# Performance work log

Measured on AMD Instinct MI355X. Metric: run time of the kernel, lower is better.

Reference implementation:

```python
import jax, jax.numpy as jnp
import numpy as np

N_NODES = 100000


def gcn_conv(x, edge_index, W, b, n_nodes):
    """PyG GCNConv: linear -> add self-loops -> symmetric-normalized scatter-sum -> bias."""
    h = x @ W  # [N, F_out]
    loop = jnp.arange(n_nodes, dtype=edge_index.dtype)
    src = jnp.concatenate([edge_index[0], loop])
    dst = jnp.concatenate([edge_index[1], loop])
    # degree of destination nodes (self-loops included)
    deg = jax.ops.segment_sum(jnp.ones_like(dst, dtype=h.dtype), dst, num_segments=n_nodes)
    dinv = jnp.where(deg > 0, jax.lax.rsqrt(deg), 0.0)
    norm = dinv[src] * dinv[dst]  # [E+N]
    msg = h[src] * norm[:, None]  # gather + scale
    out = jax.ops.segment_sum(msg, dst, num_segments=n_nodes)  # scatter-add
    return out + b


def setup_inputs() -> dict:
    key = jax.random.key(0)
    k1, k2, k3, k4 = jax.random.split(key, 4)
    d_in, hidden, out = 128, 256, 64
    x = jax.random.normal(k1, (N_NODES, d_in), dtype=jnp.float32)
    edge_index = jax.random.randint(k2, (2, 800000), 0, N_NODES, dtype=jnp.int64)
    W1 = jax.random.normal(k3, (d_in, hidden), dtype=jnp.float32) * (1.0 / np.sqrt(d_in))
    b1 = jnp.zeros((hidden,), dtype=jnp.float32)
    W2 = jax.random.normal(k4, (hidden, out), dtype=jnp.float32) * (1.0 / np.sqrt(hidden))
    b2 = jnp.zeros((out,), dtype=jnp.float32)
    return {"x": x, "edge_index": edge_index, "W1": W1, "b1": b1, "W2": W2, "b2": b2}


def reference(x, edge_index, W1, b1, W2, b2):
    h = jax.nn.relu(gcn_conv(x, edge_index, W1, b1, N_NODES))
    # dropout p=0 (module default) -> identity
    return gcn_conv(h, edge_index, W2, b2, N_NODES)
```

## Files before the change

### kernel.cpp

```cpp
#include <hip/hip_runtime.h>
#include <hip/hip_bf16.h>

#define N_NODES 100000
#define D_IN 128
#define HID 256
#define D_OUT 64
#define TR 32
#define NBUK 196
#define BSH 9

typedef __attribute__((ext_vector_type(8))) short bf8;
typedef __attribute__((ext_vector_type(4))) float f4;

static __device__ __forceinline__ unsigned short f2bf(float f) {
    __hip_bfloat16 h = __float2bfloat16(f);
    return *reinterpret_cast<unsigned short*>(&h);
}
static __device__ __forceinline__ float bflo(unsigned int u) { return __uint_as_float(u << 16); }
static __device__ __forceinline__ float bfhi(unsigned int u) { return __uint_as_float(u & 0xffff0000u); }

static __device__ __forceinline__ void fma8(float* a, float w, uint4 u) {
    a[0] += w * bflo(u.x); a[1] += w * bfhi(u.x);
    a[2] += w * bflo(u.y); a[3] += w * bfhi(u.y);
    a[4] += w * bflo(u.z); a[5] += w * bfhi(u.z);
    a[6] += w * bflo(u.w); a[7] += w * bfhi(u.w);
}
static __device__ __forceinline__ void fma4(float* a, float w, uint2 u) {
    a[0] += w * bflo(u.x); a[1] += w * bfhi(u.x);
    a[2] += w * bflo(u.y); a[3] += w * bfhi(u.y);
}


__global__ __launch_bounds__(256) void k_prep(const float* __restrict__ x,
                                              unsigned long long* __restrict__ xb,
                                              const float* __restrict__ W1,
                                              unsigned short* __restrict__ W1t,
                                              const float* __restrict__ W2,
                                              unsigned short* __restrict__ W2t,
                                              const int* __restrict__ dst, int E,
                                              int* __restrict__ hist2d) {
    int b = blockIdx.x, t = threadIdx.x;
    if (b < 12500) {
        int i = b * 256 + t;
        float4 v = ((const float4*)x)[i];
        unsigned long long o = (unsigned long long)f2bf(v.x) |
                               ((unsigned long long)f2bf(v.y) << 16) |
                               ((unsigned long long)f2bf(v.z) << 32) |
                               ((unsigned long long)f2bf(v.w) << 48);
        xb[i] = o;
    } else if (b < 12628) {
        int i = (b - 12500) * 256 + t;
        int n = i >> 7, k = i & 127;
        W1t[i] = f2bf(W1[k * HID + n]);
    } else if (b < 12692) {
        int i = (b - 12628) * 256 + t;
        int n = i >> 8, k = i & 255;
        W2t[i] = f2bf(W2[k * D_OUT + n]);
    } else {
        int hb = b - 12692;
        __shared__ int h[NBUK];
        if (t < NBUK) h[t] = 0;
        __syncthreads();
        int base = hb * 4096;
        for (int j = 0; j < 16; j++) {
            int e = base + j * 256 + t;
            if (e < E) atomicAdd(&h[dst[e] >> BSH], 1);
        }
        __syncthreads();
        if (t < NBUK) hist2d[hb * NBUK + t] = h[t];
    }
}


__global__ __launch_bounds__(256) void k_scanB1(const int* __restrict__ hist2d,
                                                int* __restrict__ blockbase,
                                                int* __restrict__ bsumB, int nbb) {
    __shared__ int s[256];
    int u = blockIdx.x, t = threadIdx.x;
    int v = (t < nbb) ? hist2d[t * NBUK + u] : 0;
    s[t] = v;
    __syncthreads();
    for (int off = 1; off < 256; off <<= 1) {
        int w = (t >= off) ? s[t - off] : 0;
        __syncthreads();
        s[t] += w;
        __syncthreads();
    }
    if (t < nbb) blockbase[t * NBUK + u] = s[t] - v;
    if (t == 255) bsumB[u] = s[255];
}

static __device__ __forceinline__ void bucket_scan(const int* __restrict__ bsumB,
                                                   int* s, int* exs, int t) {
    int v = (t < NBUK) ? bsumB[t] : 0;
    s[t] = v;
    __syncthreads();
    for (int off = 1; off < 256; off <<= 1) {
        int w = (t >= off) ? s[t - off] : 0;
        __syncthreads();
        s[t] += w;
        __syncthreads();
    }
    if (t < NBUK) exs[t] = s[t] - v;
    if (t == NBUK - 1) exs[NBUK] = s[t];
    __syncthreads();
}


__global__ __launch_bounds__(256) void k_bin(const int* __restrict__ src,
                                             const int* __restrict__ dst, int E,
                                             const int* __restrict__ blockbase,
                                             const int* __restrict__ bsumB,
                                             unsigned int* __restrict__ bin) {
    __shared__ int s[256], exs[NBUK + 1];
    __shared__ int baseL[NBUK], rankL[NBUK];
    int t = threadIdx.x;
    bucket_scan(bsumB, s, exs, t);
    if (t < NBUK) {
        baseL[t] = exs[t] + blockbase[blockIdx.x * NBUK + t];
        rankL[t] = 0;
    }
    __syncthreads();
    int base = blockIdx.x * 4096;
    for (int j = 0; j < 16; j++) {
        int e = base + j * 256 + t;
        if (e < E) {
            int sv = src[e], d = dst[e];
            int bu = d >> BSH;
            int r = atomicAdd(&rankL[bu], 1);
            bin[baseL[bu] + r] = ((unsigned int)(d & 511) << 17) | (unsigned int)sv;
        }
    }
}


__global__ __launch_bounds__(256) void k_cntscan(const unsigned int* __restrict__ bin,
                                                 const int* __restrict__ bsumB,
                                                 int* __restrict__ row_ptr,
                                                 float* __restrict__ dinv) {
    __shared__ int sb[256], exs[NBUK + 1];
    __shared__ int c[512];
    __shared__ int s[256];
    int b = blockIdx.x, t = threadIdx.x;
    bucket_scan(bsumB, sb, exs, t);
    int lo = exs[b], hi = exs[b + 1];
    c[t] = 0;
    c[t + 256] = 0;
    __syncthreads();
    for (int e = lo + t; e < hi; e += 256) atomicAdd(&c[bin[e] >> 17], 1);
    __syncthreads();
    int a0 = c[2 * t], a1 = c[2 * t + 1];
    s[t] = a0 + a1;
    __syncthreads();
    for (int off = 1; off < 256; off <<= 1) {
        int u = (t >= off) ? s[t - off] : 0;
        __syncthreads();
        s[t] += u;
        __syncthreads();
    }
    int ex = (t > 0) ? s[t - 1] : 0;
    int n0 = (b << BSH) + 2 * t;
    if (n0 < N_NODES) {
        row_ptr[n0] = lo + ex;
        dinv[n0] = rsqrtf((float)a0 + 1.0f);
    }
    if (n0 + 1 < N_NODES) {
        row_ptr[n0 + 1] = lo + ex + a0;
        dinv[n0 + 1] = rsqrtf((float)a1 + 1.0f);
    }
    if (b == NBUK - 1 && t == 255) row_ptr[N_NODES] = exs[NBUK];
}


__global__ __launch_bounds__(256) void k_place(const unsigned int* __restrict__ bin,
                                               const int* __restrict__ bsumB,
                                               const int* __restrict__ row_ptr,
                                               const float* __restrict__ dinv,
                                               int2* __restrict__ cw) {
    __shared__ int sb[256], exs[NBUK + 1];
    __shared__ int cur[512];
    __shared__ float dl[512];
    int b = blockIdx.x, t = threadIdx.x;
    bucket_scan(bsumB, sb, exs, t);
    int node0 = b << BSH;
    int nbn = N_NODES - node0;
    if (nbn > 512) nbn = 512;
    if (t < nbn) {
        cur[t] = row_ptr[node0 + t];
        dl[t] = dinv[node0 + t];
    }
    if (t + 256 < nbn) {
        cur[t + 256] = row_ptr[node0 + t + 256];
        dl[t + 256] = dinv[node0 + t + 256];
    }
    __syncthreads();
    int lo = exs[b], hi = exs[b + 1];
    for (int e = lo + t; e < hi; e += 256) {
        unsigned int rec = bin[e];
        int sv = rec & 0x1FFFF;
        int dloc = rec >> 17;
        int pos = atomicAdd(&cur[dloc], 1);
        int2 v;
        v.x = sv;
        v.y = __float_as_int(dinv[sv] * dl[dloc]);
        cw[pos] = v;
    }
}


__global__ __launch_bounds__(256) void k_pull1m(const int* __restrict__ row_ptr,
                                                const int2* __restrict__ cw,
                                                const uint4* __restrict__ xb4,
                                                const float* __restrict__ dinv,
                                                const unsigned short* __restrict__ W1t,
                                                const float* __restrict__ b1,
                                                const unsigned short* __restrict__ W2t,
                                                unsigned short* __restrict__ mb) {
    __shared__ char sA[TR * 256];
    __shared__ char sH[TR * 512];
    int t = threadIdx.x, wave = t >> 6, lane = t & 63;
    int g = lane >> 4, l = lane & 15;
    size_t row0 = (size_t)blockIdx.x * TR;

    for (int r = 0; r < 2; r++) {
        int row = r * 16 + wave * 4 + g;
        int node = (int)row0 + row;
        int beg = row_ptr[node], end = row_ptr[node + 1];
        float di = dinv[node];
        float a[8] = {0, 0, 0, 0, 0, 0, 0, 0};
        fma8(a, di * di, xb4[(size_t)node * 16 + l]);
        int e = beg;
        if (e + 4 <= end) {
            int2 c0 = cw[e], c1 = cw[e + 1], c2 = cw[e + 2], c3 = cw[e + 3];
            uint4 u0 = xb4[(size_t)c0.x * 16 + l];
            uint4 u1 = xb4[(size_t)c1.x * 16 + l];
            uint4 u2 = xb4[(size_t)c2.x * 16 + l];
            uint4 u3 = xb4[(size_t)c3.x * 16 + l];
            e += 4;
            for (; e + 4 <= end; e += 4) {
                int2 d0 = cw[e], d1 = cw[e + 1], d2 = cw[e + 2], d3 = cw[e + 3];
                uint4 v0 = xb4[(size_t)d0.x * 16 + l];
                uint4 v1 = xb4[(size_t)d1.x * 16 + l];
                uint4 v2 = xb4[(size_t)d2.x * 16 + l];
                uint4 v3 = xb4[(size_t)d3.x * 16 + l];
                fma8(a, __int_as_float(c0.y), u0);
                fma8(a, __int_as_float(c1.y), u1);
                fma8(a, __int_as_float(c2.y), u2);
                fma8(a, __int_as_float(c3.y), u3);
                c0 = d0; c1 = d1; c2 = d2; c3 = d3;
                u0 = v0; u1 = v1; u2 = v2; u3 = v3;
            }
            fma8(a, __int_as_float(c0.y), u0);
            fma8(a, __int_as_float(c1.y), u1);
            fma8(a, __int_as_float(c2.y), u2);
            fma8(a, __int_as_float(c3.y), u3);
        }
        for (; e < end; e++) {
            int2 c = cw[e];
            fma8(a, __int_as_float(c.y), xb4[(size_t)c.x * 16 + l]);
        }
        uint4 o;
        o.x = (unsigned int)f2bf(a[0]) | ((unsigned int)f2bf(a[1]) << 16);
        o.y = (unsigned int)f2bf(a[2]) | ((unsigned int)f2bf(a[3]) << 16);
        o.z = (unsigned int)f2bf(a[4]) | ((unsigned int)f2bf(a[5]) << 16);
        o.w = (unsigned int)f2bf(a[6]) | ((unsigned int)f2bf(a[7]) << 16);
        *(uint4*)(sA + ((row * 256 + l * 16) ^ ((row & 7) << 4))) = o;
    }
    __syncthreads();

    int lr = lane & 15, lg = lane >> 4;
#pragma unroll
    for (int th = 0; th < 2; th++) {
        bf8 w1f[4][2];
#pragma unroll
        for (int kk = 0; kk < 4; kk++)
#pragma unroll
            for (int q = 0; q < 2; q++)
                w1f[kk][q] = *(const bf8*)(W1t + (size_t)(wave * 64 + (th * 2 + q) * 16 + lr) * D_IN + kk * 32 + lg * 8);
        f4 acc[2][2];
#pragma unroll
        for (int q = 0; q < 2; q++) {
            acc[q][0] = (f4){0.f, 0.f, 0.f, 0.f};
            acc[q][1] = (f4){0.f, 0.f, 0.f, 0.f};
        }
#pragma unroll
        for (int kk = 0; kk < 4; kk++) {
            bf8 a0 = *(const bf8*)(sA + ((lr * 256 + kk * 64 + lg * 16) ^ ((lr & 7) << 4)));
            bf8 a1 = *(const bf8*)(sA + (((16 + lr) * 256 + kk * 64 + lg * 16) ^ (((16 + lr) & 7) << 4)));
#pragma unroll
            for (int q = 0; q < 2; q++) {
                acc[q][0] = __builtin_amdgcn_mfma_f32_16x16x32_bf16(a0, w1f[kk][q], acc[q][0], 0, 0, 0);
                acc[q][1] = __builtin_amdgcn_mfma_f32_16x16x32_bf16(a1, w1f[kk][q], acc[q][1], 0, 0, 0);
            }
        }
#pragma unroll
        for (int q = 0; q < 2; q++) {
            int colc = wave * 64 + (th * 2 + q) * 16 + lr;
            float bias = b1[colc];
#pragma unroll
            for (int h = 0; h < 2; h++) {
#pragma unroll
                for (int ri = 0; ri < 4; ri++) {
                    int row = h * 16 + lg * 4 + ri;
                    float hv = acc[q][h][ri] + bias;
                    hv = hv > 0.f ? hv : 0.f;
                    *(unsigned short*)(sH + ((row * 512 + colc * 2) ^ ((row & 7) << 4))) = f2bf(hv);
                }
            }
        }
    }
    __syncthreads();

    bf8 w2f[8];
#pragma unroll
    for (int kk = 0; kk < 8; kk++)
        w2f[kk] = *(const bf8*)(W2t + (size_t)(wave * 16 + lr) * HID + kk * 32 + lg * 8);
    f4 acc2[2];
    acc2[0] = (f4){0.f, 0.f, 0.f, 0.f};
    acc2[1] = (f4){0.f, 0.f, 0.f, 0.f};
#pragma unroll
    for (int kk = 0; kk < 8; kk++) {
        bf8 a0 = *(const bf8*)(sH + ((lr * 512 + kk * 64 + lg * 16) ^ ((lr & 7) << 4)));
        bf8 a1 = *(const bf8*)(sH + (((16 + lr) * 512 + kk * 64 + lg * 16) ^ (((16 + lr) & 7) << 4)));
        acc2[0] = __builtin_amdgcn_mfma_f32_16x16x32_bf16(a0, w2f[kk], acc2[0], 0, 0, 0);
        acc2[1] = __builtin_amdgcn_mfma_f32_16x16x32_bf16(a1, w2f[kk], acc2[1], 0, 0, 0);
    }
    int colc = wave * 16 + lr;
#pragma unroll
    for (int h = 0; h < 2; h++)
#pragma unroll
        for (int ri = 0; ri < 4; ri++) {
            int row = h * 16 + lg * 4 + ri;
            mb[(row0 + row) * D_OUT + colc] = f2bf(acc2[h][ri]);
        }
}


__global__ __launch_bounds__(256) void k_pull2(const int* __restrict__ row_ptr,
                                               const int2* __restrict__ cw,
                                               const uint2* __restrict__ m2,
                                               const float* __restrict__ dinv,
                                               const float* __restrict__ b2,
                                               float4* __restrict__ out4) {
    int wave = (blockIdx.x * 256 + threadIdx.x) >> 6;
    int lane = threadIdx.x & 63;
    int g = lane >> 4, l = lane & 15;
    int node = wave * 4 + g;
    int beg = row_ptr[node], end = row_ptr[node + 1];
    float di = dinv[node];
    float a[4] = {0, 0, 0, 0};
    fma4(a, di * di, m2[(size_t)node * 16 + l]);
    int e = beg;
    if (e + 4 <= end) {
        int2 c0 = cw[e], c1 = cw[e + 1], c2 = cw[e + 2], c3 = cw[e + 3];
        uint2 u0 = m2[(size_t)c0.x * 16 + l];
        uint2 u1 = m2[(size_t)c1.x * 16 + l];
        uint2 u2 = m2[(size_t)c2.x * 16 + l];
        uint2 u3 = m2[(size_t)c3.x * 16 + l];
        e += 4;
        for (; e + 4 <= end; e += 4) {
            int2 d0 = cw[e], d1 = cw[e + 1], d2 = cw[e + 2], d3 = cw[e + 3];
            uint2 v0 = m2[(size_t)d0.x * 16 + l];
            uint2 v1 = m2[(size_t)d1.x * 16 + l];
            uint2 v2 = m2[(size_t)d2.x * 16 + l];
            uint2 v3 = m2[(size_t)d3.x * 16 + l];
            fma4(a, __int_as_float(c0.y), u0);
            fma4(a, __int_as_float(c1.y), u1);
            fma4(a, __int_as_float(c2.y), u2);
            fma4(a, __int_as_float(c3.y), u3);
            c0 = d0; c1 = d1; c2 = d2; c3 = d3;
            u0 = v0; u1 = v1; u2 = v2; u3 = v3;
        }
        fma4(a, __int_as_float(c0.y), u0);
        fma4(a, __int_as_float(c1.y), u1);
        fma4(a, __int_as_float(c2.y), u2);
        fma4(a, __int_as_float(c3.y), u3);
    }
    for (; e < end; e++) {
        int2 c = cw[e];
        fma4(a, __int_as_float(c.y), m2[(size_t)c.x * 16 + l]);
    }
    float4 bv = ((const float4*)b2)[l];
    float4 o;
    o.x = a[0] + bv.x;
    o.y = a[1] + bv.y;
    o.z = a[2] + bv.z;
    o.w = a[3] + bv.w;
    out4[(size_t)node * 16 + l] = o;
}


extern "C" void kernel_launch(void* const* d_in, const int* in_sizes, int n_in,
                              void* d_out, int out_size, void* d_ws, size_t ws_size,
                              hipStream_t stream) {
    const float* x  = (const float*)d_in[0];
    const int*   ei = (const int*)d_in[1];
    const float* W1 = (const float*)d_in[2];
    const float* b1 = (const float*)d_in[3];
    const float* W2 = (const float*)d_in[4];
    const float* b2 = (const float*)d_in[5];
    float* out = (float*)d_out;

    const int E = in_sizes[1] / 2;
    const int* src = ei;
    const int* dst = ei + E;

    char* ws = (char*)d_ws;
    int* row_ptr        = (int*)(ws + 0);
    int2* cw            = (int2*)(ws + 400640);
    float* dinv         = (float*)(ws + 6800640);
    unsigned short* W1t = (unsigned short*)(ws + 7201024);
    unsigned short* W2t = (unsigned short*)(ws + 7266560);
    unsigned short* xb  = (unsigned short*)(ws + 7299328);
    unsigned short* mb  = (unsigned short*)(ws + 32899328);
    unsigned int* bin   = (unsigned int*)mb;
    int* hist2d         = (int*)((char*)mb + 3200256);
    int* blockbase      = (int*)((char*)mb + 3354112);
    int* bsumB          = (int*)((char*)mb + 3507968);

    const int NBB = (E + 4095) / 4096;

    k_prep<<<12692 + NBB, 256, 0, stream>>>(x, (unsigned long long*)xb, W1, W1t, W2, W2t,
                                            dst, E, hist2d);
    k_scanB1<<<NBUK, 256, 0, stream>>>(hist2d, blockbase, bsumB, NBB);
    k_bin<<<NBB, 256, 0, stream>>>(src, dst, E, blockbase, bsumB, bin);
    k_cntscan<<<NBUK, 256, 0, stream>>>(bin, bsumB, row_ptr, dinv);
    k_place<<<NBUK, 256, 0, stream>>>(bin, bsumB, row_ptr, dinv, cw);
    k_pull1m<<<3125, 256, 0, stream>>>(row_ptr, cw, (const uint4*)xb, dinv, W1t, b1, W2t, mb);
    k_pull2<<<6250, 256, 0, stream>>>(row_ptr, cw, (const uint2*)mb, dinv, b2, (float4*)out);
}
```

Baseline: 154.2 us.

## Split gather from MFMA stage and run persistent MFMA kernel reusing weights

The fused gather+MLP kernel is split in two. A standalone aggregation kernel writes bf16 aggregates to global memory, and a persistent MFMA kernel with 625 blocks loads W1/W2 fragments once and loops over five 32-row tiles, writing its 64-wide output in place into the 128-wide aggregate buffer. The gather loops are also rewritten as branchless 4-edge batches with masked weights, so there is no scalar tail loop. This trades an extra global round trip of the aggregates, plus an extra launch, for higher gather occupancy and fewer weight reloads.

```diff
diff --git a/kernel.cpp b/kernel.cpp
--- a/kernel.cpp
+++ b/kernel.cpp
@@ -8,6 +8,7 @@
 #define TR 32
 #define NBUK 196
 #define BSH 9
+#define MGRID 625
 
 typedef __attribute__((ext_vector_type(8))) short bf8;
 typedef __attribute__((ext_vector_type(4))) float f4;
@@ -28,6 +29,31 @@
 static __device__ __forceinline__ void fma4(float* a, float w, uint2 u) {
     a[0] += w * bflo(u.x); a[1] += w * bfhi(u.x);
     a[2] += w * bflo(u.y); a[3] += w * bfhi(u.y);
+}
+
+static __device__ __forceinline__ void loadb4(const int2* __restrict__ cw,
+                                              const uint4* __restrict__ xb4,
+                                              int e, int end, int beg, int l,
+                                              float* w, uint4* u) {
+#pragma unroll
+    for (int j = 0; j < 4; j++) {
+        int ej = (e + j < end) ? e + j : beg;
+        int2 c = cw[ej];
+        w[j] = (e + j < end) ? __int_as_float(c.y) : 0.f;
+        u[j] = xb4[(size_t)c.x * 16 + l];
+    }
+}
+static __device__ __forceinline__ void loadb2(const int2* __restrict__ cw,
+                                              const uint2* __restrict__ m2,
+                                              int e, int end, int beg, int l,
+                                              float* w, uint2* u) {
+#pragma unroll
+    for (int j = 0; j < 4; j++) {
+        int ej = (e + j < end) ? e + j : beg;
+        int2 c = cw[ej];
+        w[j] = (e + j < end) ? __int_as_float(c.y) : 0.f;
+        u[j] = m2[(size_t)c.x * 32 + l];
+    }
 }
 
 
@@ -208,131 +234,131 @@
 }
 
 
-__global__ __launch_bounds__(256) void k_pull1m(const int* __restrict__ row_ptr,
-                                                const int2* __restrict__ cw,
-                                                const uint4* __restrict__ xb4,
-                                                const float* __restrict__ dinv,
-                                                const unsigned short* __restrict__ W1t,
-                                                const float* __restrict__ b1,
-                                                const unsigned short* __restrict__ W2t,
-                                                unsigned short* __restrict__ mb) {
-    __shared__ char sA[TR * 256];
-    __shared__ char sH[TR * 512];
+__global__ __launch_bounds__(256) void k_pull1(const int* __restrict__ row_ptr,
+                                               const int2* __restrict__ cw,
+                                               const uint4* __restrict__ xb4,
+                                               const float* __restrict__ dinv,
+                                               uint4* __restrict__ agg4) {
+    int wave = (blockIdx.x * 256 + threadIdx.x) >> 6;
+    int lane = threadIdx.x & 63;
+    int g = lane >> 4, l = lane & 15;
+    int node = wave * 4 + g;
+    int beg = row_ptr[node], end = row_ptr[node + 1];
+    float di = dinv[node];
+    float a[8] = {0, 0, 0, 0, 0, 0, 0, 0};
+    fma8(a, di * di, xb4[(size_t)node * 16 + l]);
+    int cnt = end - beg;
+    if (cnt > 0) {
+        int nb = (cnt + 3) >> 2;
+        float w[4];
+        uint4 u[4];
+        loadb4(cw, xb4, beg, end, beg, l, w, u);
+        for (int b = 1; b < nb; b++) {
+            float nw[4];
+            uint4 nu[4];
+            loadb4(cw, xb4, beg + b * 4, end, beg, l, nw, nu);
+            fma8(a, w[0], u[0]);
+            fma8(a, w[1], u[1]);
+            fma8(a, w[2], u[2]);
+            fma8(a, w[3], u[3]);
+#pragma unroll
+            for (int j = 0; j < 4; j++) {
+                w[j] = nw[j];
+                u[j] = nu[j];
+            }
+        }
+        fma8(a, w[0], u[0]);
+        fma8(a, w[1], u[1]);
+        fma8(a, w[2], u[2]);
+        fma8(a, w[3], u[3]);
+    }
+    uint4 o;
+    o.x = (unsigned int)f2bf(a[0]) | ((unsigned int)f2bf(a[1]) << 16);
+    o.y = (unsigned int)f2bf(a[2]) | ((unsigned int)f2bf(a[3]) << 16);
+    o.z = (unsigned int)f2bf(a[4]) | ((unsigned int)f2bf(a[5]) << 16);
+    o.w = (unsigned int)f2bf(a[6]) | ((unsigned int)f2bf(a[7]) << 16);
+    agg4[(size_t)node * 16 + l] = o;
+}
+
+
+__global__ __launch_bounds__(256) void k_fused_mfma(unsigned short* __restrict__ agg,
+                                                    const unsigned short* __restrict__ W1t,
+                                                    const float* __restrict__ b1,
+                                                    const unsigned short* __restrict__ W2t) {
+    __shared__ char sH[TR * HID * 2];
     int t = threadIdx.x, wave = t >> 6, lane = t & 63;
-    int g = lane >> 4, l = lane & 15;
-    size_t row0 = (size_t)blockIdx.x * TR;
-
-    for (int r = 0; r < 2; r++) {
-        int row = r * 16 + wave * 4 + g;
-        int node = (int)row0 + row;
-        int beg = row_ptr[node], end = row_ptr[node + 1];
-        float di = dinv[node];
-        float a[8] = {0, 0, 0, 0, 0, 0, 0, 0};
-        fma8(a, di * di, xb4[(size_t)node * 16 + l]);
-        int e = beg;
-        if (e + 4 <= end) {
-            int2 c0 = cw[e], c1 = cw[e + 1], c2 = cw[e + 2], c3 = cw[e + 3];
-            uint4 u0 = xb4[(size_t)c0.x * 16 + l];
-            uint4 u1 = xb4[(size_t)c1.x * 16 + l];
-            uint4 u2 = xb4[(size_t)c2.x * 16 + l];
-            uint4 u3 = xb4[(size_t)c3.x * 16 + l];
-            e += 4;
-            for (; e + 4 <= end; e += 4) {
-                int2 d0 = cw[e], d1 = cw[e + 1], d2 = cw[e + 2], d3 = cw[e + 3];
-                uint4 v0 = xb4[(size_t)d0.x * 16 + l];
-                uint4 v1 = xb4[(size_t)d1.x * 16 + l];
-                uint4 v2 = xb4[(size_t)d2.x * 16 + l];
-                uint4 v3 = xb4[(size_t)d3.x * 16 + l];
-                fma8(a, __int_as_float(c0.y), u0);
-                fma8(a, __int_as_float(c1.y), u1);
-                fma8(a, __int_as_float(c2.y), u2);
-                fma8(a, __int_as_float(c3.y), u3);
-                c0 = d0; c1 = d1; c2 = d2; c3 = d3;
-                u0 = v0; u1 = v1; u2 = v2; u3 = v3;
+    int lr = lane & 15, lg = lane >> 4;
+
+    bf8 w1f[4][4];
+#pragma unroll
+    for (int kk = 0; kk < 4; kk++)
+#pragma unroll
+        for (int tt = 0; tt < 4; tt++)
+            w1f[kk][tt] = *(const bf8*)(W1t + (size_t)(wave * 64 + tt * 16 + lr) * D_IN + kk * 32 + lg * 8);
+    bf8 w2f[8];
+#pragma unroll
+    for (int kk = 0; kk < 8; kk++)
+        w2f[kk] = *(const bf8*)(W2t + (size_t)(wave * 16 + lr) * HID + kk * 32 + lg * 8);
+    float bias[4];
+#pragma unroll
+    for (int tt = 0; tt < 4; tt++) bias[tt] = b1[wave * 64 + tt * 16 + lr];
+
+    for (int it = 0; it < 5; it++) {
+        size_t row0 = ((size_t)blockIdx.x + (size_t)it * MGRID) * TR;
+
+        f4 acc1[4][2];
+#pragma unroll
+        for (int tt = 0; tt < 4; tt++)
+#pragma unroll
+            for (int h = 0; h < 2; h++) acc1[tt][h] = (f4){0.f, 0.f, 0.f, 0.f};
+
+#pragma unroll
+        for (int kk = 0; kk < 4; kk++) {
+            bf8 a0 = *(const bf8*)(agg + (row0 + lr) * 128 + kk * 32 + lg * 8);
+            bf8 a1 = *(const bf8*)(agg + (row0 + 16 + lr) * 128 + kk * 32 + lg * 8);
+#pragma unroll
+            for (int tt = 0; tt < 4; tt++) {
+                acc1[tt][0] = __builtin_amdgcn_mfma_f32_16x16x32_bf16(a0, w1f[kk][tt], acc1[tt][0], 0, 0, 0);
+                acc1[tt][1] = __builtin_amdgcn_mfma_f32_16x16x32_bf16(a1, w1f[kk][tt], acc1[tt][1], 0, 0, 0);
             }
-            fma8(a, __int_as_float(c0.y), u0);
-            fma8(a, __int_as_float(c1.y), u1);
-            fma8(a, __int_as_float(c2.y), u2);
-            fma8(a, __int_as_float(c3.y), u3);
-        }
-        for (; e < end; e++) {
-            int2 c = cw[e];
-            fma8(a, __int_as_float(c.y), xb4[(size_t)c.x * 16 + l]);
-        }
-        uint4 o;
-        o.x = (unsigned int)f2bf(a[0]) | ((unsigned int)f2bf(a[1]) << 16);
-        o.y = (unsigned int)f2bf(a[2]) | ((unsigned int)f2bf(a[3]) << 16);
-        o.z = (unsigned int)f2bf(a[4]) | ((unsigned int)f2bf(a[5]) << 16);
-        o.w = (unsigned int)f2bf(a[6]) | ((unsigned int)f2bf(a[7]) << 16);
-        *(uint4*)(sA + ((row * 256 + l * 16) ^ ((row & 7) << 4))) = o;
-    }
-    __syncthreads();
-
-    int lr = lane & 15, lg = lane >> 4;
-#pragma unroll
-    for (int th = 0; th < 2; th++) {
-        bf8 w1f[4][2];
-#pragma unroll
-        for (int kk = 0; kk < 4; kk++)
-#pragma unroll
-            for (int q = 0; q < 2; q++)
-                w1f[kk][q] = *(const bf8*)(W1t + (size_t)(wave * 64 + (th * 2 + q) * 16 + lr) * D_IN + kk * 32 + lg * 8);
-        f4 acc[2][2];
-#pragma unroll
-        for (int q = 0; q < 2; q++) {
-            acc[q][0] = (f4){0.f, 0.f, 0.f, 0.f};
-            acc[q][1] = (f4){0.f, 0.f, 0.f, 0.f};
-        }
-#pragma unroll
-        for (int kk = 0; kk < 4; kk++) {
-            bf8 a0 = *(const bf8*)(sA + ((lr * 256 + kk * 64 + lg * 16) ^ ((lr & 7) << 4)));
-            bf8 a1 = *(const bf8*)(sA + (((16 + lr) * 256 + kk * 64 + lg * 16) ^ (((16 + lr) & 7) << 4)));
-#pragma unroll
-            for (int q = 0; q < 2; q++) {
-                acc[q][0] = __builtin_amdgcn_mfma_f32_16x16x32_bf16(a0, w1f[kk][q], acc[q][0], 0, 0, 0);
-                acc[q][1] = __builtin_amdgcn_mfma_f32_16x16x32_bf16(a1, w1f[kk][q], acc[q][1], 0, 0, 0);
-            }
-        }
-#pragma unroll
-        for (int q = 0; q < 2; q++) {
-            int colc = wave * 64 + (th * 2 + q) * 16 + lr;
-            float bias = b1[colc];
+        }
+
+#pragma unroll
+        for (int tt = 0; tt < 4; tt++) {
+            int colc = wave * 64 + tt * 16 + lr;
 #pragma unroll
             for (int h = 0; h < 2; h++) {
 #pragma unroll
                 for (int ri = 0; ri < 4; ri++) {
                     int row = h * 16 + lg * 4 + ri;
-                    float hv = acc[q][h][ri] + bias;
+                    float hv = acc1[tt][h][ri] + bias[tt];
                     hv = hv > 0.f ? hv : 0.f;
                     *(unsigned short*)(sH + ((row * 512 + colc * 2) ^ ((row & 7) << 4))) = f2bf(hv);
                 }
             }
         }
-    }
-    __syncthreads();
-
-    bf8 w2f[8];
-#pragma unroll
-    for (int kk = 0; kk < 8; kk++)
-        w2f[kk] = *(const bf8*)(W2t + (size_t)(wave * 16 + lr) * HID + kk * 32 + lg * 8);
-    f4 acc2[2];
-    acc2[0] = (f4){0.f, 0.f, 0.f, 0.f};
-    acc2[1] = (f4){0.f, 0.f, 0.f, 0.f};
-#pragma unroll
-    for (int kk = 0; kk < 8; kk++) {
-        bf8 a0 = *(const bf8*)(sH + ((lr * 512 + kk * 64 + lg * 16) ^ ((lr & 7) << 4)));
-        bf8 a1 = *(const bf8*)(sH + (((16 + lr) * 512 + kk * 64 + lg * 16) ^ (((16 + lr) & 7) << 4)));
-        acc2[0] = __builtin_amdgcn_mfma_f32_16x16x32_bf16(a0, w2f[kk], acc2[0], 0, 0, 0);
-        acc2[1] = __builtin_amdgcn_mfma_f32_16x16x32_bf16(a1, w2f[kk], acc2[1], 0, 0, 0);
-    }
-    int colc = wave * 16 + lr;
-#pragma unroll
-    for (int h = 0; h < 2; h++)
-#pragma unroll
-        for (int ri = 0; ri < 4; ri++) {
-            int row = h * 16 + lg * 4 + ri;
-            mb[(row0 + row) * D_OUT + colc] = f2bf(acc2[h][ri]);
-        }
+        __syncthreads();
+
+        f4 acc2[2];
+        acc2[0] = (f4){0.f, 0.f, 0.f, 0.f};
+        acc2[1] = (f4){0.f, 0.f, 0.f, 0.f};
+#pragma unroll
+        for (int kk = 0; kk < 8; kk++) {
+            bf8 a0 = *(const bf8*)(sH + ((lr * 512 + kk * 64 + lg * 16) ^ ((lr & 7) << 4)));
+            bf8 a1 = *(const bf8*)(sH + (((16 + lr) * 512 + kk * 64 + lg * 16) ^ (((16 + lr) & 7) << 4)));
+            acc2[0] = __builtin_amdgcn_mfma_f32_16x16x32_bf16(a0, w2f[kk], acc2[0], 0, 0, 0);
+            acc2[1] = __builtin_amdgcn_mfma_f32_16x16x32_bf16(a1, w2f[kk], acc2[1], 0, 0, 0);
+        }
+        int colc = wave * 16 + lr;
+#pragma unroll
+        for (int h = 0; h < 2; h++)
+#pragma unroll
+            for (int ri = 0; ri < 4; ri++) {
+                int row = h * 16 + lg * 4 + ri;
+                agg[(row0 + row) * 128 + colc] = f2bf(acc2[h][ri]);
+            }
+        __syncthreads();
+    }
 }
 
 
@@ -349,36 +375,31 @@
     int beg = row_ptr[node], end = row_ptr[node + 1];
     float di = dinv[node];
     float a[4] = {0, 0, 0, 0};
-    fma4(a, di * di, m2[(size_t)node * 16 + l]);
-    int e = beg;
-    if (e + 4 <= end) {
-        int2 c0 = cw[e], c1 = cw[e + 1], c2 = cw[e + 2], c3 = cw[e + 3];
-        uint2 u0 = m2[(size_t)c0.x * 16 + l];
-        uint2 u1 = m2[(size_t)c1.x * 16 + l];
-        uint2 u2 = m2[(size_t)c2.x * 16 + l];
-        uint2 u3 = m2[(size_t)c3.x * 16 + l];
-        e += 4;
-        for (; e + 4 <= end; e += 4) {
-            int2 d0 = cw[e], d1 = cw[e + 1], d2 = cw[e + 2], d3 = cw[e + 3];
-            uint2 v0 = m2[(size_t)d0.x * 16 + l];
-            uint2 v1 = m2[(size_t)d1.x * 16 + l];
-            uint2 v2 = m2[(size_t)d2.x * 16 + l];
-            uint2 v3 = m2[(size_t)d3.x * 16 + l];
-            fma4(a, __int_as_float(c0.y), u0);
-            fma4(a, __int_as_float(c1.y), u1);
-            fma4(a, __int_as_float(c2.y), u2);
-            fma4(a, __int_as_float(c3.y), u3);
-            c0 = d0; c1 = d1; c2 = d2; c3 = d3;
-            u0 = v0; u1 = v1; u2 = v2; u3 = v3;
-        }
-        fma4(a, __int_as_float(c0.y), u0);
-        fma4(a, __int_as_float(c1.y), u1);
-        fma4(a, __int_as_float(c2.y), u2);
-        fma4(a, __int_as_float(c3.y), u3);
-    }
-    for (; e < end; e++) {
-        int2 c = cw[e];
-        fma4(a, __int_as_float(c.y), m2[(size_t)c.x * 16 + l]);
+    fma4(a, di * di, m2[(size_t)node * 32 + l]);
+    int cnt = end - beg;
+    if (cnt > 0) {
+        int nb = (cnt + 3) >> 2;
+        float w[4];
+        uint2 u[4];
+        loadb2(cw, m2, beg, end, beg, l, w, u);
+        for (int b = 1; b < nb; b++) {
+            float nw[4];
+            uint2 nu[4];
+            loadb2(cw, m2, beg + b * 4, end, beg, l, nw, nu);
+            fma4(a, w[0], u[0]);
+            fma4(a, w[1], u[1]);
+            fma4(a, w[2], u[2]);
+            fma4(a, w[3], u[3]);
+#pragma unroll
+            for (int j = 0; j < 4; j++) {
+                w[j] = nw[j];
+                u[j] = nu[j];
+            }
+        }
+        fma4(a, w[0], u[0]);
+        fma4(a, w[1], u[1]);
+        fma4(a, w[2], u[2]);
+        fma4(a, w[3], u[3]);
     }
     float4 bv = ((const float4*)b2)[l];
     float4 o;
@@ -412,11 +433,11 @@
     unsigned short* W1t = (unsigned short*)(ws + 7201024);
     unsigned short* W2t = (unsigned short*)(ws + 7266560);
     unsigned short* xb  = (unsigned short*)(ws + 7299328);
-    unsigned short* mb  = (unsigned short*)(ws + 32899328);
-    unsigned int* bin   = (unsigned int*)mb;
-    int* hist2d         = (int*)((char*)mb + 3200256);
-    int* blockbase      = (int*)((char*)mb + 3354112);
-    int* bsumB          = (int*)((char*)mb + 3507968);
+    unsigned short* aggb = (unsigned short*)(ws + 32899328);
+    unsigned int* bin   = (unsigned int*)aggb;
+    int* hist2d         = (int*)((char*)aggb + 3200256);
+    int* blockbase      = (int*)((char*)aggb + 3354112);
+    int* bsumB          = (int*)((char*)aggb + 3507968);
 
     const int NBB = (E + 4095) / 4096;
 
@@ -426,6 +447,7 @@
     k_bin<<<NBB, 256, 0, stream>>>(src, dst, E, blockbase, bsumB, bin);
     k_cntscan<<<NBUK, 256, 0, stream>>>(bin, bsumB, row_ptr, dinv);
     k_place<<<NBUK, 256, 0, stream>>>(bin, bsumB, row_ptr, dinv, cw);
-    k_pull1m<<<3125, 256, 0, stream>>>(row_ptr, cw, (const uint4*)xb, dinv, W1t, b1, W2t, mb);
-    k_pull2<<<6250, 256, 0, stream>>>(row_ptr, cw, (const uint2*)mb, dinv, b2, (float4*)out);
-}
+    k_pull1<<<6250, 256, 0, stream>>>(row_ptr, cw, (const uint4*)xb, dinv, (uint4*)aggb);
+    k_fused_mfma<<<MGRID, 256, 0, stream>>>(aggb, W1t, b1, W2t);
+    k_pull2<<<6250, 256, 0, stream>>>(row_ptr, cw, (const uint2*)aggb, dinv, b2, (float4*)out);
+}
```

After: 162.0 us. +5.1%, slower.
